# Kernel optimization log

Measured on AMD Instinct MI355X. Metric: run time of the kernel, lower is better.

## Reference

```python
import jax, jax.numpy as jnp
import numpy as np

EPS = 1e-08
SIGMA = 0.1
B = 1.0


def setup_inputs() -> dict:
    key = jax.random.key(0)
    k1, k2 = jax.random.split(key)
    N, C, H, W = 4, 256, 64, 64
    featureT = jax.random.normal(k1, (N, C, H, W), dtype=jnp.float32)
    featureI = jax.random.normal(k2, (N, C, H, W), dtype=jnp.float32)
    return {"featureT": featureT, "featureI": featureI}


def reference(featureT, featureI):
    N, C, H, W = featureT.shape
    # center both by target mean over (batch, spatial)
    meanT = featureT.mean(axis=(0, 2, 3), keepdims=True)
    fI = featureI - meanT
    fT = featureT - meanT
    # channel-wise L2 normalize
    fI = fI / (jnp.linalg.norm(fI, axis=1, keepdims=True) + EPS)
    fT = fT / (jnp.linalg.norm(fT, axis=1, keepdims=True) + EPS)
    # 1x1-patch conv2d == contraction over channels: sim[n, p, h, w]
    # where p indexes the flattened H*W spatial positions of the target.
    fT_flat = fT.reshape(N, C, H * W)  # [N, C, P]
    sim = jnp.einsum('nchw,ncp->nphw', fI, fT_flat)  # [N, P, H, W]
    raw_dist = (1.0 - sim) / 2.0
    # relative distances: divide by min over patch axis
    div = jnp.min(raw_dist, axis=1, keepdims=True)
    relative_dist = raw_dist / (div + EPS)
    # contextual similarity: exp-weight + sum-normalize over patch axis
    Wt = jnp.exp((B - relative_dist) / (SIGMA + EPS))
    W_sum = Wt.sum(axis=1, keepdims=True)
    CX = Wt / (W_sum + EPS)
    # max over spatial dims of featureI, mean over patches, -log, mean over batch
    CX = CX.max(axis=(2, 3))           # [N, P]
    CX = CX.mean(axis=1)               # [N]
    CX_loss = -jnp.log(CX + EPS)
    return jnp.mean(CX_loss)
```

## Files before the change

kernel.cpp:

```cpp
#include <hip/hip_runtime.h>
#include <cmath>


#define NB 4
#define CC 256
#define HW 4096
#define NQ0 8
#define NCS 16

static constexpr float kEPS = 1e-8f;
static constexpr float kSIG = 0.1f + 1e-8f;

typedef __attribute__((ext_vector_type(8)))  short short8;
typedef __attribute__((ext_vector_type(16))) float f32x16;

enum {
  OFF_MEAN = 0,
  OFF_CMAX = 256,
  OFF_WSUM = OFF_CMAX + NQ0*NB*HW,
  OFF_MAXP = OFF_WSUM + NQ0*NB*HW,
  OFF_MAXV = OFF_MAXP + NCS*NB*HW,
  OFF_GT   = OFF_MAXV + NB*HW,
  OFF_GI   = OFF_GT + NB*HW*CC/2,
  WS_FLOATS_FULL = OFF_GI + NB*HW*CC/2
};

__device__ __forceinline__ ushort cvt_bf16(float x) {
  unsigned u = __float_as_uint(x);
  unsigned r = (u + 0x7fffu + ((u >> 16) & 1u)) >> 16;
  return (ushort)r;
}

__device__ __forceinline__ void glds16(const ushort* g, ushort* l) {
  __builtin_amdgcn_global_load_lds(
      (const __attribute__((address_space(1))) unsigned*)g,
      (__attribute__((address_space(3))) unsigned*)l, 16, 0, 0);
}

__device__ __forceinline__ float blockSum256(float v) {
  __shared__ float sh[4];
  const int lane = threadIdx.x & 63, wv = threadIdx.x >> 6;
  #pragma unroll
  for (int o = 32; o > 0; o >>= 1) v += __shfl_down(v, o, 64);
  __syncthreads();
  if (lane == 0) sh[wv] = v;
  __syncthreads();
  return sh[0] + sh[1] + sh[2] + sh[3];
}

__global__ __launch_bounds__(256) void k_mean9(const float* __restrict__ fT,
                                               float* __restrict__ ws) {
  const int c = blockIdx.x, t = threadIdx.x;
  float s = 0.f;
  for (int n = 0; n < NB; ++n) {
    const float* p = fT + (size_t)(n*CC + c)*HW;
    #pragma unroll
    for (int k = 0; k < 16; ++k) s += p[k*256 + t];
  }
  const float tot = blockSum256(s);
  if (t == 0) ws[OFF_MEAN + c] = tot * (1.0f/16384.0f);
}

__global__ __launch_bounds__(256) void k_prep9(const float* __restrict__ fT,
                                               const float* __restrict__ fI,
                                               float* __restrict__ ws) {
  __shared__ float stage[32][257];
  __shared__ float prt[8][32];
  __shared__ float sinv[32];
  const int t = threadIdx.x, l = t & 63;
  int bid = blockIdx.x;
  const int tensor = (bid >= 512); bid &= 511;
  const int n   = bid >> 7;
  const int r32 = bid & 127;
  const int p0  = r32 * 32;

  const float* __restrict__ src = tensor ? fI : fT;
  ushort* __restrict__ dst = (ushort*)(ws + (tensor ? OFF_GI : OFF_GT));
  const float* __restrict__ mean = ws + OFF_MEAN;

  const int pl = t & 31, cg = t >> 5;
  float acc = 0.f;
  #pragma unroll
  for (int i = 0; i < 32; ++i) {
    const int c = cg*32 + i;
    const float v = src[((size_t)(n*CC + c))*HW + p0 + pl] - mean[c];
    stage[pl][c] = v;
    acc += v*v;
  }
  prt[cg][pl] = acc;
  __syncthreads();
  if (t < 32) {
    float s = 0.f;
    #pragma unroll
    for (int g = 0; g < 8; ++g) s += prt[g][t];
    sinv[t] = 1.0f/(sqrtf(s) + kEPS);
  }
  __syncthreads();

  const int w = t >> 6, lhi = l >> 5, m = l & 31;
  const float iv = sinv[m];
  #pragma unroll
  for (int i = 0; i < 4; ++i) {
    const int kc = w*4 + i;
    const int cb = kc*16 + lhi*8;
    short8 o;
    #pragma unroll
    for (int j = 0; j < 8; ++j)
      ((ushort*)&o)[j] = cvt_bf16(stage[m][cb + j] * iv);
    *(short8*)(dst + (((size_t)(n*128 + r32)*16 + kc) << 9) + l*8) = o;
  }
}


#define SWEEP_PROLOGUE                                                        \
  const int t = threadIdx.x;                                                  \
  const int w = t >> 6, l = t & 63;                                           \
  const int ln31 = l & 31, lhi = l >> 5;  (void)lhi;                          \
  const int L = blockIdx.x;                                                   \
  const int xcd = L & 7, g = L >> 3;                                          \
  const int nh = xcd*4 + (g & 3);                                             \
  const int cs = g >> 2;                                                      \
  const int n = nh >> 3, h = nh & 7;                                          \
  const int col0 = cs * 256;

#define LOAD_BREG                                                             \
  short8 breg0[16], breg1[16];                                                \
  {                                                                           \
    const int RB0 = cs*8 + w, RB1 = cs*8 + 4 + w;                             \
    _Pragma("unroll")                                                         \
    for (int kc = 0; kc < 16; ++kc) {                                         \
      breg0[kc] = *(const short8*)(gB + (((size_t)(n*128 + RB0)*16 + kc) << 9) + l*8); \
      breg1[kc] = *(const short8*)(gB + (((size_t)(n*128 + RB1)*16 + kc) << 9) + l*8); \
    }                                                                         \
  }

#define STAGE_TILE(it_, buf_)                                                 \
  {                                                                           \
    const ushort* __restrict__ srcg = gAn + (size_t)(it_)*16384;              \
    ushort* __restrict__ dstl = &Ab[buf_][0];                                 \
    _Pragma("unroll")                                                         \
    for (int i = 0; i < 8; ++i)                                               \
      glds16(srcg + (size_t)(i*256 + t)*8, dstl + (i*256 + t)*8);             \
  }

#define MFMA_ITER(buf_)                                                       \
  f32x16 acc00, acc01, acc10, acc11;                                          \
  _Pragma("unroll")                                                           \
  for (int e = 0; e < 16; ++e) { acc00[e]=0.f; acc01[e]=0.f; acc10[e]=0.f; acc11[e]=0.f; } \
  {                                                                           \
    const ushort* __restrict__ Abuf = &Ab[buf_][0];                           \
    _Pragma("unroll")                                                         \
    for (int kc = 0; kc < 16; ++kc) {                                         \
      const short8 a0 = *(const short8*)&Abuf[kc*512 + l*8];                  \
      const short8 a1 = *(const short8*)&Abuf[8192 + kc*512 + l*8];           \
      acc00 = __builtin_amdgcn_mfma_f32_32x32x16_bf16(a0, breg0[kc], acc00, 0, 0, 0); \
      acc01 = __builtin_amdgcn_mfma_f32_32x32x16_bf16(a0, breg1[kc], acc01, 0, 0, 0); \
      acc10 = __builtin_amdgcn_mfma_f32_32x32x16_bf16(a1, breg0[kc], acc10, 0, 0, 0); \
      acc11 = __builtin_amdgcn_mfma_f32_32x32x16_bf16(a1, breg1[kc], acc11, 0, 0, 0); \
    }                                                                         \
  }

__global__ __launch_bounds__(256, 2) void k_gA(
    const ushort* __restrict__ gA, const ushort* __restrict__ gB,
    float* __restrict__ ws)
{
  __shared__ ushort Ab[2][16384];
  __shared__ float red2[256];

  SWEEP_PROLOGUE
  const ushort* __restrict__ gAn = gA + ((size_t)(n*128 + h*16) << 13);

  STAGE_TILE(0, 0)
  LOAD_BREG

  float run0 = -3.0e38f, run1 = -3.0e38f;

  for (int it = 0; it < 8; ++it) {
    __syncthreads();
    if (it + 1 < 8) STAGE_TILE(it + 1, (it + 1) & 1)

    MFMA_ITER(it & 1)

    #pragma unroll
    for (int r = 0; r < 16; ++r) {
      run0 = fmaxf(run0, fmaxf(acc00[r], acc10[r]));
      run1 = fmaxf(run1, fmaxf(acc01[r], acc11[r]));
    }
  }

  run0 = fmaxf(run0, __shfl_xor(run0, 32, 64));
  run1 = fmaxf(run1, __shfl_xor(run1, 32, 64));
  if (l < 32) {
    red2[w*32 + ln31]       = run0;
    red2[128 + w*32 + ln31] = run1;
  }
  __syncthreads();
  ws[OFF_CMAX + h*(NB*HW) + n*HW + col0 + t] = red2[t];
}

__global__ __launch_bounds__(256, 2) void k_gB(
    const ushort* __restrict__ gA, const ushort* __restrict__ gB,
    float* __restrict__ ws)
{
  __shared__ ushort Ab[2][16384];
  __shared__ float red2[256];

  SWEEP_PROLOGUE
  const ushort* __restrict__ gAn = gA + ((size_t)(n*128 + h*16) << 13);

  STAGE_TILE(0, 0)

  float aq0, bq0, aq1, bq1;
  {
    const int q0 = col0 + w*32 + ln31;
    const int q1 = q0 + 128;
    float cm0 = -3.0e38f, cm1 = -3.0e38f;
    #pragma unroll
    for (int hh = 0; hh < NQ0; ++hh) {
      cm0 = fmaxf(cm0, ws[OFF_CMAX + hh*(NB*HW) + n*HW + q0]);
      cm1 = fmaxf(cm1, ws[OFF_CMAX + hh*(NB*HW) + n*HW + q1]);
    }
    const float i0 = 1.0f/(2.0f*(0.5f*(1.0f - cm0) + kEPS));
    const float i1 = 1.0f/(2.0f*(0.5f*(1.0f - cm1) + kEPS));
    bq0 = i0 / kSIG; aq0 = (1.0f - i0) / kSIG;
    bq1 = i1 / kSIG; aq1 = (1.0f - i1) / kSIG;
  }

  LOAD_BREG

  float ws0 = 0.f, ws1 = 0.f;

  for (int it = 0; it < 8; ++it) {
    __syncthreads();
    if (it + 1 < 8) STAGE_TILE(it + 1, (it + 1) & 1)

    MFMA_ITER(it & 1)

    #pragma unroll
    for (int r = 0; r < 16; ++r) {
      ws0 += __expf(fmaf(bq0, acc00[r], aq0));
      ws0 += __expf(fmaf(bq0, acc10[r], aq0));
      ws1 += __expf(fmaf(bq1, acc01[r], aq1));
      ws1 += __expf(fmaf(bq1, acc11[r], aq1));
    }
  }

  ws0 += __shfl_xor(ws0, 32, 64);
  ws1 += __shfl_xor(ws1, 32, 64);
  if (l < 32) {
    red2[w*32 + ln31]       = ws0;
    red2[128 + w*32 + ln31] = ws1;
  }
  __syncthreads();
  ws[OFF_WSUM + h*(NB*HW) + n*HW + col0 + t] = red2[t];
}

__global__ __launch_bounds__(256, 2) void k_gC(
    const ushort* __restrict__ gA, const ushort* __restrict__ gB,
    float* __restrict__ ws)
{
  __shared__ ushort Ab[2][16384];
  __shared__ float stash[4][512];

  SWEEP_PROLOGUE
  const ushort* __restrict__ gAn = gA + ((size_t)(n*128 + h*16) << 13);

  STAGE_TILE(0, 0)

  float gq0, bq0, gq1, bq1;
  {
    const int q0 = col0 + w*32 + ln31;
    const int q1 = q0 + 128;
    float cm0 = -3.0e38f, cm1 = -3.0e38f;
    #pragma unroll
    for (int hh = 0; hh < NQ0; ++hh) {
      cm0 = fmaxf(cm0, ws[OFF_CMAX + hh*(NB*HW) + n*HW + q0]);
      cm1 = fmaxf(cm1, ws[OFF_CMAX + hh*(NB*HW) + n*HW + q1]);
    }
    float sw0 = 0.f, sw1 = 0.f;
    #pragma unroll
    for (int hh = 0; hh < NQ0; ++hh) {
      sw0 += ws[OFF_WSUM + hh*(NB*HW) + n*HW + q0];
      sw1 += ws[OFF_WSUM + hh*(NB*HW) + n*HW + q1];
    }
    const float i0 = 1.0f/(2.0f*(0.5f*(1.0f - cm0) + kEPS));
    const float i1 = 1.0f/(2.0f*(0.5f*(1.0f - cm1) + kEPS));
    bq0 = i0 / kSIG;
    bq1 = i1 / kSIG;
    gq0 = (1.0f - i0) / kSIG - logf(sw0 + kEPS);
    gq1 = (1.0f - i1) / kSIG - logf(sw1 + kEPS);
  }

  LOAD_BREG

  for (int it = 0; it < 8; ++it) {
    __syncthreads();
    if (it + 1 < 8) STAGE_TILE(it + 1, (it + 1) & 1)

    MFMA_ITER(it & 1)

    #pragma unroll
    for (int r = 0; r < 16; ++r) {
      float v0 = fmaxf(fmaf(bq0, acc00[r], gq0), fmaf(bq1, acc01[r], gq1));
      float v1 = fmaxf(fmaf(bq0, acc10[r], gq0), fmaf(bq1, acc11[r], gq1));
      #pragma unroll
      for (int o = 1; o <= 16; o <<= 1) {
        v0 = fmaxf(v0, __shfl_xor(v0, o, 64));
        v1 = fmaxf(v1, __shfl_xor(v1, o, 64));
      }
      if (ln31 == 0) {
        const int pl = it*64 + 4*lhi + (r & 3) + 8*(r >> 2);
        stash[w][pl]      = v0;
        stash[w][pl + 32] = v1;
      }
    }
  }

  __syncthreads();
  float* __restrict__ MAXP = ws + OFF_MAXP + (size_t)cs*(NB*HW) + n*HW + h*512;
  #pragma unroll
  for (int p = t; p < 512; p += 256) {
    const float m = fmaxf(fmaxf(stash[0][p], stash[1][p]),
                          fmaxf(stash[2][p], stash[3][p]));
    MAXP[p] = m;
  }
}

__global__ __launch_bounds__(256) void k_red(float* __restrict__ ws) {
  const int idx = blockIdx.x*256 + threadIdx.x;
  float m = ws[OFF_MAXP + idx];
  #pragma unroll
  for (int s = 1; s < NCS; ++s)
    m = fmaxf(m, ws[OFF_MAXP + s*(NB*HW) + idx]);
  ws[OFF_MAXV + idx] = m;
}

__global__ __launch_bounds__(256) void k_final9(const float* __restrict__ ws,
                                                float* __restrict__ out) {
  const int t = threadIdx.x;
  float loss = 0.f;
  for (int n = 0; n < NB; ++n) {
    float s = 0.f;
    for (int k = 0; k < 16; ++k)
      s += __expf(ws[OFF_MAXV + n*HW + k*256 + t]);
    const float tot = blockSum256(s);
    loss += -logf(tot*(1.0f/4096.0f) + kEPS);
  }
  if (t == 0) out[0] = loss*0.25f;
}

extern "C" void kernel_launch(void* const* d_in, const int* in_sizes, int n_in,
                              void* d_out, int out_size, void* d_ws, size_t ws_size,
                              hipStream_t stream) {
  const float* fT = (const float*)d_in[0];
  const float* fI = (const float*)d_in[1];
  float* out = (float*)d_out;
  float* ws  = (float*)d_ws;

  const size_t need_full = (size_t)WS_FLOATS_FULL * sizeof(float);
  if (ws_size < need_full) return;

  const ushort* GT = (const ushort*)(ws + OFF_GT);
  const ushort* GI = (const ushort*)(ws + OFF_GI);
  k_mean9 <<<256,  256, 0, stream>>>(fT, ws);
  k_prep9 <<<1024, 256, 0, stream>>>(fT, fI, ws);
  k_gA    <<<512,  256, 0, stream>>>(GT, GI, ws);
  k_gB    <<<512,  256, 0, stream>>>(GT, GI, ws);
  k_gC    <<<512,  256, 0, stream>>>(GT, GI, ws);
  k_red   <<<64,   256, 0, stream>>>(ws);
  k_final9<<<1,    256, 0, stream>>>(ws, out);
}
```

Before: 200.9 us.

## Deepen LDS prefetch with manual waitcnt barriers and transpose MFMA in gC reduction

All three sweep kernels now prefetch two A tiles ahead into the double buffer. They synchronise with explicit s_waitcnt vmcnt/lgkmcnt and s_barrier instead of __syncthreads, so the next global-to-LDS copy overlaps more MFMA work. In k_gC the MFMA operands are swapped so each lane holds its output column in registers. This replaces the per-row 5-step shuffle max reduction with an in-register max plus a single cross-half shuffle, with the per-row scale and offset read from shared memory. The raw inline-asm waits depend on the exact count of outstanding loads, and the lds-staged gam/bet reads add LDS traffic.

```diff
diff --git a/kernel.cpp b/kernel.cpp
--- a/kernel.cpp
+++ b/kernel.cpp
@@ -36,6 +36,10 @@
       (const __attribute__((address_space(1))) unsigned*)g,
       (__attribute__((address_space(3))) unsigned*)l, 16, 0, 0);
 }
+__device__ __forceinline__ void s_bar()  { asm volatile("s_barrier" ::: "memory"); }
+__device__ __forceinline__ void w_vm8()  { asm volatile("s_waitcnt vmcnt(8)" ::: "memory"); }
+__device__ __forceinline__ void w_vm0()  { asm volatile("s_waitcnt vmcnt(0)" ::: "memory"); }
+__device__ __forceinline__ void w_lgkm() { asm volatile("s_waitcnt lgkmcnt(0)" ::: "memory"); }
 
 __device__ __forceinline__ float blockSum256(float v) {
   __shared__ float sh[4];
@@ -112,7 +116,7 @@
 }
 
 
-#define SWEEP_PROLOGUE                                                        \
+#define SWEEP_IDS                                                             \
   const int t = threadIdx.x;                                                  \
   const int w = t >> 6, l = t & 63;                                           \
   const int ln31 = l & 31, lhi = l >> 5;  (void)lhi;                          \
@@ -136,28 +140,11 @@
 
 #define STAGE_TILE(it_, buf_)                                                 \
   {                                                                           \
-    const ushort* __restrict__ srcg = gAn + (size_t)(it_)*16384;              \
+    const ushort* __restrict__ srcg = gAn + ((size_t)(it_) << 14);            \
     ushort* __restrict__ dstl = &Ab[buf_][0];                                 \
     _Pragma("unroll")                                                         \
     for (int i = 0; i < 8; ++i)                                               \
       glds16(srcg + (size_t)(i*256 + t)*8, dstl + (i*256 + t)*8);             \
-  }
-
-#define MFMA_ITER(buf_)                                                       \
-  f32x16 acc00, acc01, acc10, acc11;                                          \
-  _Pragma("unroll")                                                           \
-  for (int e = 0; e < 16; ++e) { acc00[e]=0.f; acc01[e]=0.f; acc10[e]=0.f; acc11[e]=0.f; } \
-  {                                                                           \
-    const ushort* __restrict__ Abuf = &Ab[buf_][0];                           \
-    _Pragma("unroll")                                                         \
-    for (int kc = 0; kc < 16; ++kc) {                                         \
-      const short8 a0 = *(const short8*)&Abuf[kc*512 + l*8];                  \
-      const short8 a1 = *(const short8*)&Abuf[8192 + kc*512 + l*8];           \
-      acc00 = __builtin_amdgcn_mfma_f32_32x32x16_bf16(a0, breg0[kc], acc00, 0, 0, 0); \
-      acc01 = __builtin_amdgcn_mfma_f32_32x32x16_bf16(a0, breg1[kc], acc01, 0, 0, 0); \
-      acc10 = __builtin_amdgcn_mfma_f32_32x32x16_bf16(a1, breg0[kc], acc10, 0, 0, 0); \
-      acc11 = __builtin_amdgcn_mfma_f32_32x32x16_bf16(a1, breg1[kc], acc11, 0, 0, 0); \
-    }                                                                         \
   }
 
 __global__ __launch_bounds__(256, 2) void k_gA(
@@ -167,19 +154,35 @@
   __shared__ ushort Ab[2][16384];
   __shared__ float red2[256];
 
-  SWEEP_PROLOGUE
+  SWEEP_IDS
   const ushort* __restrict__ gAn = gA + ((size_t)(n*128 + h*16) << 13);
 
   STAGE_TILE(0, 0)
+  STAGE_TILE(1, 1)
   LOAD_BREG
 
   float run0 = -3.0e38f, run1 = -3.0e38f;
 
   for (int it = 0; it < 8; ++it) {
-    __syncthreads();
-    if (it + 1 < 8) STAGE_TILE(it + 1, (it + 1) & 1)
-
-    MFMA_ITER(it & 1)
+    if (it < 7) w_vm8(); else w_vm0();
+    s_bar();
+
+    const ushort* __restrict__ Abuf = &Ab[it & 1][0];
+    f32x16 acc00, acc01, acc10, acc11;
+    #pragma unroll
+    for (int e = 0; e < 16; ++e) { acc00[e]=0.f; acc01[e]=0.f; acc10[e]=0.f; acc11[e]=0.f; }
+    #pragma unroll
+    for (int kc = 0; kc < 16; ++kc) {
+      const short8 a0 = *(const short8*)&Abuf[kc*512 + l*8];
+      const short8 a1 = *(const short8*)&Abuf[8192 + kc*512 + l*8];
+      acc00 = __builtin_amdgcn_mfma_f32_32x32x16_bf16(a0, breg0[kc], acc00, 0, 0, 0);
+      acc01 = __builtin_amdgcn_mfma_f32_32x32x16_bf16(a0, breg1[kc], acc01, 0, 0, 0);
+      acc10 = __builtin_amdgcn_mfma_f32_32x32x16_bf16(a1, breg0[kc], acc10, 0, 0, 0);
+      acc11 = __builtin_amdgcn_mfma_f32_32x32x16_bf16(a1, breg1[kc], acc11, 0, 0, 0);
+    }
+    w_lgkm();
+    s_bar();
+    if (it + 2 < 8) STAGE_TILE(it + 2, it & 1)
 
     #pragma unroll
     for (int r = 0; r < 16; ++r) {
@@ -205,10 +208,11 @@
   __shared__ ushort Ab[2][16384];
   __shared__ float red2[256];
 
-  SWEEP_PROLOGUE
+  SWEEP_IDS
   const ushort* __restrict__ gAn = gA + ((size_t)(n*128 + h*16) << 13);
 
   STAGE_TILE(0, 0)
+  STAGE_TILE(1, 1)
 
   float aq0, bq0, aq1, bq1;
   {
@@ -231,10 +235,25 @@
   float ws0 = 0.f, ws1 = 0.f;
 
   for (int it = 0; it < 8; ++it) {
-    __syncthreads();
-    if (it + 1 < 8) STAGE_TILE(it + 1, (it + 1) & 1)
-
-    MFMA_ITER(it & 1)
+    if (it < 7) w_vm8(); else w_vm0();
+    s_bar();
+
+    const ushort* __restrict__ Abuf = &Ab[it & 1][0];
+    f32x16 acc00, acc01, acc10, acc11;
+    #pragma unroll
+    for (int e = 0; e < 16; ++e) { acc00[e]=0.f; acc01[e]=0.f; acc10[e]=0.f; acc11[e]=0.f; }
+    #pragma unroll
+    for (int kc = 0; kc < 16; ++kc) {
+      const short8 a0 = *(const short8*)&Abuf[kc*512 + l*8];
+      const short8 a1 = *(const short8*)&Abuf[8192 + kc*512 + l*8];
+      acc00 = __builtin_amdgcn_mfma_f32_32x32x16_bf16(a0, breg0[kc], acc00, 0, 0, 0);
+      acc01 = __builtin_amdgcn_mfma_f32_32x32x16_bf16(a0, breg1[kc], acc01, 0, 0, 0);
+      acc10 = __builtin_amdgcn_mfma_f32_32x32x16_bf16(a1, breg0[kc], acc10, 0, 0, 0);
+      acc11 = __builtin_amdgcn_mfma_f32_32x32x16_bf16(a1, breg1[kc], acc11, 0, 0, 0);
+    }
+    w_lgkm();
+    s_bar();
+    if (it + 2 < 8) STAGE_TILE(it + 2, it & 1)
 
     #pragma unroll
     for (int r = 0; r < 16; ++r) {
@@ -260,59 +279,70 @@
     float* __restrict__ ws)
 {
   __shared__ ushort Ab[2][16384];
+  __shared__ float gam_s[256], bet_s[256];
   __shared__ float stash[4][512];
 
-  SWEEP_PROLOGUE
+  SWEEP_IDS
   const ushort* __restrict__ gAn = gA + ((size_t)(n*128 + h*16) << 13);
 
   STAGE_TILE(0, 0)
-
-  float gq0, bq0, gq1, bq1;
+  STAGE_TILE(1, 1)
+
   {
-    const int q0 = col0 + w*32 + ln31;
-    const int q1 = q0 + 128;
-    float cm0 = -3.0e38f, cm1 = -3.0e38f;
-    #pragma unroll
-    for (int hh = 0; hh < NQ0; ++hh) {
-      cm0 = fmaxf(cm0, ws[OFF_CMAX + hh*(NB*HW) + n*HW + q0]);
-      cm1 = fmaxf(cm1, ws[OFF_CMAX + hh*(NB*HW) + n*HW + q1]);
-    }
-    float sw0 = 0.f, sw1 = 0.f;
-    #pragma unroll
-    for (int hh = 0; hh < NQ0; ++hh) {
-      sw0 += ws[OFF_WSUM + hh*(NB*HW) + n*HW + q0];
-      sw1 += ws[OFF_WSUM + hh*(NB*HW) + n*HW + q1];
-    }
-    const float i0 = 1.0f/(2.0f*(0.5f*(1.0f - cm0) + kEPS));
-    const float i1 = 1.0f/(2.0f*(0.5f*(1.0f - cm1) + kEPS));
-    bq0 = i0 / kSIG;
-    bq1 = i1 / kSIG;
-    gq0 = (1.0f - i0) / kSIG - logf(sw0 + kEPS);
-    gq1 = (1.0f - i1) / kSIG - logf(sw1 + kEPS);
+    const int idx = n*HW + col0 + t;
+    float cm = -3.0e38f;
+    #pragma unroll
+    for (int hh = 0; hh < NQ0; ++hh)
+      cm = fmaxf(cm, ws[OFF_CMAX + hh*(NB*HW) + idx]);
+    float sw = 0.f;
+    #pragma unroll
+    for (int hh = 0; hh < NQ0; ++hh)
+      sw += ws[OFF_WSUM + hh*(NB*HW) + idx];
+    const float i0 = 1.0f/(2.0f*(0.5f*(1.0f - cm) + kEPS));
+    bet_s[t] = i0 / kSIG;
+    gam_s[t] = (1.0f - i0) / kSIG - logf(sw + kEPS);
   }
 
   LOAD_BREG
+  __syncthreads();
 
   for (int it = 0; it < 8; ++it) {
-    __syncthreads();
-    if (it + 1 < 8) STAGE_TILE(it + 1, (it + 1) & 1)
-
-    MFMA_ITER(it & 1)
-
+    if (it < 7) w_vm8(); else w_vm0();
+    s_bar();
+
+    const ushort* __restrict__ Abuf = &Ab[it & 1][0];
+    f32x16 acc00, acc01, acc10, acc11;
+    #pragma unroll
+    for (int e = 0; e < 16; ++e) { acc00[e]=0.f; acc01[e]=0.f; acc10[e]=0.f; acc11[e]=0.f; }
+    #pragma unroll
+    for (int kc = 0; kc < 16; ++kc) {
+      const short8 a0 = *(const short8*)&Abuf[kc*512 + l*8];
+      const short8 a1 = *(const short8*)&Abuf[8192 + kc*512 + l*8];
+      acc00 = __builtin_amdgcn_mfma_f32_32x32x16_bf16(breg0[kc], a0, acc00, 0, 0, 0);
+      acc01 = __builtin_amdgcn_mfma_f32_32x32x16_bf16(breg0[kc], a1, acc01, 0, 0, 0);
+      acc10 = __builtin_amdgcn_mfma_f32_32x32x16_bf16(breg1[kc], a0, acc10, 0, 0, 0);
+      acc11 = __builtin_amdgcn_mfma_f32_32x32x16_bf16(breg1[kc], a1, acc11, 0, 0, 0);
+    }
+    w_lgkm();
+    s_bar();
+    if (it + 2 < 8) STAGE_TILE(it + 2, it & 1)
+
+    float m0 = -3.0e38f, m1 = -3.0e38f;
     #pragma unroll
     for (int r = 0; r < 16; ++r) {
-      float v0 = fmaxf(fmaf(bq0, acc00[r], gq0), fmaf(bq1, acc01[r], gq1));
-      float v1 = fmaxf(fmaf(bq0, acc10[r], gq0), fmaf(bq1, acc11[r], gq1));
-      #pragma unroll
-      for (int o = 1; o <= 16; o <<= 1) {
-        v0 = fmaxf(v0, __shfl_xor(v0, o, 64));
-        v1 = fmaxf(v1, __shfl_xor(v1, o, 64));
-      }
-      if (ln31 == 0) {
-        const int pl = it*64 + 4*lhi + (r & 3) + 8*(r >> 2);
-        stash[w][pl]      = v0;
-        stash[w][pl + 32] = v1;
-      }
+      const int row = (r & 3) + 8*(r >> 2) + 4*lhi;
+      const float g0v = gam_s[w*32 + row],       b0v = bet_s[w*32 + row];
+      const float g1v = gam_s[128 + w*32 + row], b1v = bet_s[128 + w*32 + row];
+      m0 = fmaxf(m0, fmaf(b0v, acc00[r], g0v));
+      m0 = fmaxf(m0, fmaf(b1v, acc10[r], g1v));
+      m1 = fmaxf(m1, fmaf(b0v, acc01[r], g0v));
+      m1 = fmaxf(m1, fmaf(b1v, acc11[r], g1v));
+    }
+    m0 = fmaxf(m0, __shfl_xor(m0, 32, 64));
+    m1 = fmaxf(m1, __shfl_xor(m1, 32, 64));
+    if (l < 32) {
+      stash[w][it*64 + ln31]      = m0;
+      stash[w][it*64 + 32 + ln31] = m1;
     }
   }
 
@@ -320,9 +350,8 @@
   float* __restrict__ MAXP = ws + OFF_MAXP + (size_t)cs*(NB*HW) + n*HW + h*512;
   #pragma unroll
   for (int p = t; p < 512; p += 256) {
-    const float m = fmaxf(fmaxf(stash[0][p], stash[1][p]),
-                          fmaxf(stash[2][p], stash[3][p]));
-    MAXP[p] = m;
+    MAXP[p] = fmaxf(fmaxf(stash[0][p], stash[1][p]),
+                    fmaxf(stash[2][p], stash[3][p]));
   }
 }
 
```

New measurement: 178.1 us. 1.13x faster.
